# Optimization experiments

Measured on AMD Instinct MI355X. Metric: run time of the kernel, lower is better.

## Reference

```python
import jax, jax.numpy as jnp
import numpy as np

EPS = 1e-06


def setup_inputs() -> dict:
    key = jax.random.key(0)
    k1, k2, k3 = jax.random.split(key, 3)
    B, H, S, D = 4, 16, 4096, 64
    query = jax.random.normal(k1, (B, H, S, D), dtype=jnp.float32)
    key_t = jax.random.normal(k2, (B, H, S, D), dtype=jnp.float32)
    value = jax.random.normal(k3, (B, H, S, D), dtype=jnp.float32)
    return {"query": query, "key": key_t, "value": value}


def _cosformer_features(x, cos_idx, sin_idx):
    # x: [B,H,S,D]; cos_idx/sin_idx: [S,1] -> features [B,H,S,2D]
    x_relu = jax.nn.relu(x)
    return jnp.concatenate([x_relu * cos_idx, x_relu * sin_idx], axis=-1)


def reference(query, key, value):
    B, H, S, D = query.shape
    query = query / jnp.sqrt(jnp.asarray(D, dtype=query.dtype))
    # idx = (pi/2) * [1..S]; angles divided by seq_len
    ang = (jnp.pi / 2) * jnp.arange(1, S + 1, dtype=query.dtype) / S  # [S]
    cos_idx = jnp.cos(ang)[:, None]  # [S,1]
    sin_idx = jnp.sin(ang)[:, None]  # [S,1]
    q_cs = _cosformer_features(query, cos_idx, sin_idx)  # [B,H,S,2D]
    k_cs = _cosformer_features(key, cos_idx, sin_idx)    # [B,H,S,2D]
    # norm: 1 / clamp(q_cs . sum_l(k_cs), eps)
    k_sum = jnp.sum(k_cs, axis=-2)  # [B,H,2D]
    norm = 1.0 / jnp.maximum(jnp.einsum('bhld,bhd->bhl', q_cs, k_sum), EPS)  # [B,H,S]
    # linear attention: KV aggregation then query projection
    kv = jnp.einsum('bhld,bhlm->bhdm', k_cs, value)  # [B,H,2D,D]
    out = jnp.einsum('bhld,bhdm->bhlm', q_cs, kv) * norm[..., None]  # [B,H,S,D]
    return out
```

## Files before the change

kernel.cpp:

```cpp
#include <hip/hip_runtime.h>
#include <hip/hip_bf16.h>
#include <math.h>

#define BHN    64
#define SEQ    4096
#define DIM    64
#define NCHUNK 16
#define CHUNK  (SEQ / NCHUNK)
#define KSTEP  64
#define NIT    (CHUNK / KSTEP)
#define KVF    (128 * DIM)
#define STRIDE_C ((size_t)BHN * KVF + (size_t)BHN * 128)
#define KSBASE ((size_t)BHN * KVF)
#define FRAGH  10240
#define LPAD   72

typedef __bf16 bf16x8v __attribute__((ext_vector_type(8)));
typedef float  f32x4v  __attribute__((ext_vector_type(4)));

__device__ inline f32x4v mfma16(bf16x8v a, bf16x8v b, f32x4v c) {
    return __builtin_amdgcn_mfma_f32_16x16x32_bf16(a, b, c, 0, 0, 0);
}

__device__ inline unsigned pk2(float a, float b) {
    __hip_bfloat162 t(__float2bfloat16(a), __float2bfloat16(b));
    return *(unsigned*)&t;
}

template<int USE_ATOMIC>
__global__ __launch_bounds__(256) void cosformer_kv_mfma(
    const float* __restrict__ K, const float* __restrict__ V,
    float* __restrict__ part)
{
    __shared__ ushort ktc[64][LPAD];
    __shared__ ushort kts[64][LPAD];
    __shared__ ushort vt [64][LPAD];

    const int bh    = blockIdx.x / NCHUNK;
    const int chunk = blockIdx.x % NCHUNK;
    const int row0  = chunk * CHUNK;
    const float* Kb = K + (size_t)bh * SEQ * DIM;
    const float* Vb = V + (size_t)bh * SEQ * DIM;

    const int tid  = threadIdx.x;
    const int ssub = (tid & 31) * 2;
    const int dblk = (tid >> 5) * 8;
    const int lane = tid & 63;
    const int w    = tid >> 6;
    const int frow = lane & 15;
    const int kgrp = lane >> 4;

    f32x4v acc[2][5];
    #pragma unroll
    for (int i = 0; i < 2; ++i)
        #pragma unroll
        for (int t = 0; t < 5; ++t) acc[i][t] = (f32x4v){0.f, 0.f, 0.f, 0.f};

    bf16x8v onef;
    #pragma unroll
    for (int j = 0; j < 8; ++j) onef[j] = (frow == 0) ? (__bf16)1.0f : (__bf16)0.0f;

    float4 kreg[4], vreg[4];

    auto LOADS = [&](int it) {
        const float* kp = Kb + (size_t)(row0 + it * KSTEP + ssub) * DIM + dblk;
        const float* vp = Vb + (size_t)(row0 + it * KSTEP + ssub) * DIM + dblk;
        kreg[0] = *(const float4*)kp;
        kreg[1] = *(const float4*)(kp + 4);
        kreg[2] = *(const float4*)(kp + DIM);
        kreg[3] = *(const float4*)(kp + DIM + 4);
        vreg[0] = *(const float4*)vp;
        vreg[1] = *(const float4*)(vp + 4);
        vreg[2] = *(const float4*)(vp + DIM);
        vreg[3] = *(const float4*)(vp + DIM + 4);
    };

    auto WRITES = [&](int it) {
        const int l0 = row0 + it * KSTEP + ssub;
        const float CC = 1.5707963267948966f / (float)SEQ;
        float s0v, c0, s1v, c1;
        __sincosf(CC * (float)(l0 + 1), &s0v, &c0);
        __sincosf(CC * (float)(l0 + 2), &s1v, &c1);
        float k0[8] = {kreg[0].x, kreg[0].y, kreg[0].z, kreg[0].w,
                       kreg[1].x, kreg[1].y, kreg[1].z, kreg[1].w};
        float k1[8] = {kreg[2].x, kreg[2].y, kreg[2].z, kreg[2].w,
                       kreg[3].x, kreg[3].y, kreg[3].z, kreg[3].w};
        float v0[8] = {vreg[0].x, vreg[0].y, vreg[0].z, vreg[0].w,
                       vreg[1].x, vreg[1].y, vreg[1].z, vreg[1].w};
        float v1[8] = {vreg[2].x, vreg[2].y, vreg[2].z, vreg[2].w,
                       vreg[3].x, vreg[3].y, vreg[3].z, vreg[3].w};
        #pragma unroll
        for (int i = 0; i < 8; ++i) {
            float r0 = fmaxf(k0[i], 0.f), r1 = fmaxf(k1[i], 0.f);
            *(unsigned*)&ktc[dblk + i][ssub] = pk2(r0 * c0,  r1 * c1);
            *(unsigned*)&kts[dblk + i][ssub] = pk2(r0 * s0v, r1 * s1v);
            *(unsigned*)&vt [dblk + i][ssub] = pk2(v0[i],    v1[i]);
        }
    };

    LOADS(0);
    WRITES(0);
    LOADS(1);
    __syncthreads();

    const ushort (*ap)[LPAD] = (w < 2) ? ktc : kts;
    const int d0 = ((2 * w) & 3) * 16 + frow;

    for (int it = 0; it < NIT; ++it) {
        #pragma unroll
        for (int ks = 0; ks < 2; ++ks) {
            const int so = ks * 32 + kgrp * 8;
            bf16x8v a0 = *(const bf16x8v*)&ap[d0][so];
            bf16x8v a1 = *(const bf16x8v*)&ap[d0 + 16][so];
            #pragma unroll
            for (int nt = 0; nt < 4; ++nt) {
                bf16x8v b = *(const bf16x8v*)&vt[nt * 16 + frow][so];
                acc[0][nt] = mfma16(a0, b, acc[0][nt]);
                acc[1][nt] = mfma16(a1, b, acc[1][nt]);
            }
            acc[0][4] = mfma16(a0, onef, acc[0][4]);
            acc[1][4] = mfma16(a1, onef, acc[1][4]);
        }
        __syncthreads();
        if (it + 1 < NIT) {
            WRITES(it + 1);
            if (it + 2 < NIT) LOADS(it + 2);
            __syncthreads();
        }
    }

    if (USE_ATOMIC) {
        float* pb = part + (size_t)bh * KVF;
        float* ps = part + KSBASE + bh * 128;
        #pragma unroll
        for (int mi = 0; mi < 2; ++mi) {
            const int fb = (2 * w + mi) * 16 + kgrp * 4;
            #pragma unroll
            for (int nt = 0; nt < 4; ++nt)
                #pragma unroll
                for (int r = 0; r < 4; ++r)
                    atomicAdd(&pb[(size_t)(fb + r) * DIM + nt * 16 + frow], acc[mi][nt][r]);
            if (frow == 0)
                #pragma unroll
                for (int r = 0; r < 4; ++r) atomicAdd(&ps[fb + r], acc[mi][4][r]);
        }
    } else {
        float* pb = part + STRIDE_C * chunk + (size_t)bh * KVF;
        float* ps = part + STRIDE_C * chunk + KSBASE + bh * 128;
        #pragma unroll
        for (int mi = 0; mi < 2; ++mi) {
            const int fb = (2 * w + mi) * 16 + kgrp * 4;
            #pragma unroll
            for (int nt = 0; nt < 4; ++nt)
                #pragma unroll
                for (int r = 0; r < 4; ++r)
                    pb[(size_t)(fb + r) * DIM + nt * 16 + frow] = acc[mi][nt][r];
            if (frow == 0)
                #pragma unroll
                for (int r = 0; r < 4; ++r) ps[fb + r] = acc[mi][4][r];
        }
    }
}

template<int NC>
__global__ __launch_bounds__(256) void reduce_pack(
    const float* __restrict__ part, __hip_bfloat16* __restrict__ bfrag)
{
    size_t o = (size_t)blockIdx.x * 256 + threadIdx.x;
    float s = 0.f;
    #pragma unroll
    for (int c = 0; c < NC; ++c) s += part[(size_t)c * STRIDE_C + o];
    if (o < KSBASE) {
        int head = (int)(o >> 13);
        int r = (int)(o & 8191);
        int k = r >> 6, n = r & 63;
        int t = n >> 4, ks = k >> 5, lg = (k >> 3) & 3, j = k & 7;
        int lane = lg * 16 + (n & 15);
        bfrag[(size_t)head * FRAGH + (size_t)(((t * 4 + ks) * 64 + lane) * 8 + j)] =
            __float2bfloat16(s);
    } else {
        int r = (int)(o - KSBASE);
        int head = r >> 7, k = r & 127;
        int ks = k >> 5, lg = (k >> 3) & 3, j = k & 7;
        bfrag[(size_t)head * FRAGH + (size_t)(((16 + ks) * 64 + lg * 16) * 8 + j)] =
            __float2bfloat16(s);
    }
}

__global__ __launch_bounds__(256) void cosformer_out_mfma(
    const float* __restrict__ Q, const __hip_bfloat16* __restrict__ bfrag,
    float* __restrict__ out)
{
    __shared__ __hip_bfloat16 sb[FRAGH];
    const int head = blockIdx.x >> 3;
    const int tile = blockIdx.x & 7;
    const int tid  = threadIdx.x;

    {
        const float4* src = (const float4*)(bfrag + (size_t)head * FRAGH);
        float4* dst = (float4*)sb;
        #pragma unroll
        for (int i = 0; i < 5; ++i) dst[tid + 256 * i] = src[tid + 256 * i];
    }

    const int lane = tid & 63;
    const int w    = tid >> 6;
    const int mrow = lane & 15;
    const int kgrp = lane >> 4;

    const float* Qb = Q + (size_t)head * SEQ * DIM;
    float*       Ob = out + (size_t)head * SEQ * DIM;
    const int rowblk = tile * 512;

    float4 qb[2][4];
    #pragma unroll
    for (int m = 0; m < 2; ++m) {
        const float4* qr = (const float4*)(Qb + (size_t)(rowblk + w * 32 + m * 16 + mrow) * DIM);
        qb[m][0] = qr[kgrp * 2];
        qb[m][1] = qr[kgrp * 2 + 1];
        qb[m][2] = qr[8 + kgrp * 2];
        qb[m][3] = qr[8 + kgrp * 2 + 1];
    }

    __syncthreads();

    #pragma unroll
    for (int g = 0; g < 4; ++g) {
        const int base = rowblk + (g * 4 + w) * 32;

        bf16x8v af[2][4];
        #pragma unroll
        for (int m = 0; m < 2; ++m) {
            int arow = base + m * 16 + mrow;
            float ang = 1.5707963267948966f * (float)(arow + 1) / (float)SEQ;
            float sn, cn;
            __sincosf(ang, &sn, &cn);
            float crs = cn * 0.125f, srs = sn * 0.125f;
            float lo[8] = {qb[m][0].x, qb[m][0].y, qb[m][0].z, qb[m][0].w,
                           qb[m][1].x, qb[m][1].y, qb[m][1].z, qb[m][1].w};
            float hi[8] = {qb[m][2].x, qb[m][2].y, qb[m][2].z, qb[m][2].w,
                           qb[m][3].x, qb[m][3].y, qb[m][3].z, qb[m][3].w};
            #pragma unroll
            for (int j = 0; j < 8; ++j) {
                float rl = fmaxf(lo[j], 0.f);
                float rh = fmaxf(hi[j], 0.f);
                af[m][0][j] = (__bf16)(rl * crs);
                af[m][1][j] = (__bf16)(rh * crs);
                af[m][2][j] = (__bf16)(rl * srs);
                af[m][3][j] = (__bf16)(rh * srs);
            }
        }

        if (g < 3) {
            #pragma unroll
            for (int m = 0; m < 2; ++m) {
                const float4* qr = (const float4*)(Qb + (size_t)(rowblk + ((g + 1) * 4 + w) * 32 + m * 16 + mrow) * DIM);
                qb[m][0] = qr[kgrp * 2];
                qb[m][1] = qr[kgrp * 2 + 1];
                qb[m][2] = qr[8 + kgrp * 2];
                qb[m][3] = qr[8 + kgrp * 2 + 1];
            }
        }

        f32x4v acc[2][5];
        #pragma unroll
        for (int m = 0; m < 2; ++m)
            #pragma unroll
            for (int t = 0; t < 5; ++t)
                acc[m][t] = (f32x4v){0.f, 0.f, 0.f, 0.f};

        #pragma unroll
        for (int t = 0; t < 5; ++t)
            #pragma unroll
            for (int ks = 0; ks < 4; ++ks) {
                bf16x8v bf = *(const bf16x8v*)&sb[(size_t)(((t * 4 + ks) * 64 + lane) * 8)];
                acc[0][t] = mfma16(af[0][ks], bf, acc[0][t]);
                acc[1][t] = mfma16(af[1][ks], bf, acc[1][t]);
            }

        #pragma unroll
        for (int m = 0; m < 2; ++m) {
            #pragma unroll
            for (int r = 0; r < 4; ++r) {
                float den = __shfl(acc[m][4][r], lane & 48, 64);
                float invd = 1.0f / fmaxf(den, 1e-6f);
                int row = base + m * 16 + kgrp * 4 + r;
                float* op = Ob + (size_t)row * DIM + mrow;
                op[0]  = acc[m][0][r] * invd;
                op[16] = acc[m][1][r] * invd;
                op[32] = acc[m][2][r] * invd;
                op[48] = acc[m][3][r] * invd;
            }
        }
    }
}

extern "C" void kernel_launch(void* const* d_in, const int* in_sizes, int n_in,
                              void* d_out, int out_size, void* d_ws, size_t ws_size,
                              hipStream_t stream) {
    const float* Q = (const float*)d_in[0];
    const float* K = (const float*)d_in[1];
    const float* V = (const float*)d_in[2];
    float* out = (float*)d_out;
    float* ws  = (float*)d_ws;

    const size_t frag_bytes = (size_t)FRAGH * BHN * sizeof(__hip_bfloat16);
    const size_t need_full  = (size_t)NCHUNK * STRIDE_C * sizeof(float) + frag_bytes;

    if (ws_size >= need_full) {
        float* part = ws;
        __hip_bfloat16* bfrag = (__hip_bfloat16*)(ws + (size_t)NCHUNK * STRIDE_C);
        hipMemsetAsync(bfrag, 0, frag_bytes, stream);
        hipLaunchKernelGGL((cosformer_kv_mfma<0>), dim3(BHN * NCHUNK), dim3(256), 0, stream,
                           K, V, part);
        hipLaunchKernelGGL((reduce_pack<NCHUNK>), dim3((int)(STRIDE_C / 256)), dim3(256), 0, stream,
                           part, bfrag);
        hipLaunchKernelGGL(cosformer_out_mfma, dim3(BHN * 8), dim3(256), 0, stream,
                           Q, bfrag, out);
    } else {
        float* part = ws;
        __hip_bfloat16* bfrag = (__hip_bfloat16*)(ws + STRIDE_C);
        hipMemsetAsync(part, 0, STRIDE_C * sizeof(float), stream);
        hipMemsetAsync(bfrag, 0, frag_bytes, stream);
        hipLaunchKernelGGL((cosformer_kv_mfma<1>), dim3(BHN * NCHUNK), dim3(256), 0, stream,
                           K, V, part);
        hipLaunchKernelGGL((reduce_pack<1>), dim3((int)(STRIDE_C / 256)), dim3(256), 0, stream,
                           part, bfrag);
        hipLaunchKernelGGL(cosformer_out_mfma, dim3(BHN * 8), dim3(256), 0, stream,
                           Q, bfrag, out);
    }
}
```

Measured before the change: 80.91 us.

## Double KV kernel block to 512 threads and XOR-swizzle LDS tiles

The KV aggregation kernel now runs 8 waves per block instead of 4. Each wave computes one 16-row feature tile instead of two, which halves per-thread accumulators and global loads. The transposed LDS tiles are written with an XOR swizzle on the column index, and the MFMA fragment reads use the same swizzle, to cut bank conflicts on the transposed stores. This gives more parallelism and lower register pressure per thread, at the cost of reloading each B fragment for every wave and more barrier participants.

```diff
diff --git a/kernel.cpp b/kernel.cpp
--- a/kernel.cpp
+++ b/kernel.cpp
@@ -27,8 +27,10 @@
     return *(unsigned*)&t;
 }
 
+__device__ inline int swz(int d, int col) { return col ^ (4 * ((d >> 2) & 7)); }
+
 template<int USE_ATOMIC>
-__global__ __launch_bounds__(256) void cosformer_kv_mfma(
+__global__ __launch_bounds__(512) void cosformer_kv_mfma(
     const float* __restrict__ K, const float* __restrict__ V,
     float* __restrict__ part)
 {
@@ -42,59 +44,51 @@
     const float* Kb = K + (size_t)bh * SEQ * DIM;
     const float* Vb = V + (size_t)bh * SEQ * DIM;
 
-    const int tid  = threadIdx.x;
-    const int ssub = (tid & 31) * 2;
-    const int dblk = (tid >> 5) * 8;
+    const int tid = threadIdx.x;
+    const int dq = (tid & 15) * 4;
+    const int g  = tid >> 4;
     const int lane = tid & 63;
     const int w    = tid >> 6;
     const int frow = lane & 15;
     const int kgrp = lane >> 4;
 
-    f32x4v acc[2][5];
-    #pragma unroll
-    for (int i = 0; i < 2; ++i)
-        #pragma unroll
-        for (int t = 0; t < 5; ++t) acc[i][t] = (f32x4v){0.f, 0.f, 0.f, 0.f};
+    f32x4v acc[5];
+    #pragma unroll
+    for (int t = 0; t < 5; ++t) acc[t] = (f32x4v){0.f, 0.f, 0.f, 0.f};
 
     bf16x8v onef;
     #pragma unroll
     for (int j = 0; j < 8; ++j) onef[j] = (frow == 0) ? (__bf16)1.0f : (__bf16)0.0f;
 
-    float4 kreg[4], vreg[4];
+    float4 ka, kb2, va, vb2;
 
     auto LOADS = [&](int it) {
-        const float* kp = Kb + (size_t)(row0 + it * KSTEP + ssub) * DIM + dblk;
-        const float* vp = Vb + (size_t)(row0 + it * KSTEP + ssub) * DIM + dblk;
-        kreg[0] = *(const float4*)kp;
-        kreg[1] = *(const float4*)(kp + 4);
-        kreg[2] = *(const float4*)(kp + DIM);
-        kreg[3] = *(const float4*)(kp + DIM + 4);
-        vreg[0] = *(const float4*)vp;
-        vreg[1] = *(const float4*)(vp + 4);
-        vreg[2] = *(const float4*)(vp + DIM);
-        vreg[3] = *(const float4*)(vp + DIM + 4);
+        const float* kp = Kb + (size_t)(row0 + it * KSTEP + 2 * g) * DIM + dq;
+        const float* vp = Vb + (size_t)(row0 + it * KSTEP + 2 * g) * DIM + dq;
+        ka  = *(const float4*)kp;
+        kb2 = *(const float4*)(kp + DIM);
+        va  = *(const float4*)vp;
+        vb2 = *(const float4*)(vp + DIM);
     };
 
     auto WRITES = [&](int it) {
-        const int l0 = row0 + it * KSTEP + ssub;
+        const int l0 = row0 + it * KSTEP + 2 * g;
         const float CC = 1.5707963267948966f / (float)SEQ;
         float s0v, c0, s1v, c1;
         __sincosf(CC * (float)(l0 + 1), &s0v, &c0);
         __sincosf(CC * (float)(l0 + 2), &s1v, &c1);
-        float k0[8] = {kreg[0].x, kreg[0].y, kreg[0].z, kreg[0].w,
-                       kreg[1].x, kreg[1].y, kreg[1].z, kreg[1].w};
-        float k1[8] = {kreg[2].x, kreg[2].y, kreg[2].z, kreg[2].w,
-                       kreg[3].x, kreg[3].y, kreg[3].z, kreg[3].w};
-        float v0[8] = {vreg[0].x, vreg[0].y, vreg[0].z, vreg[0].w,
-                       vreg[1].x, vreg[1].y, vreg[1].z, vreg[1].w};
-        float v1[8] = {vreg[2].x, vreg[2].y, vreg[2].z, vreg[2].w,
-                       vreg[3].x, vreg[3].y, vreg[3].z, vreg[3].w};
-        #pragma unroll
-        for (int i = 0; i < 8; ++i) {
+        float k0[4] = {ka.x, ka.y, ka.z, ka.w};
+        float k1[4] = {kb2.x, kb2.y, kb2.z, kb2.w};
+        float v0[4] = {va.x, va.y, va.z, va.w};
+        float v1[4] = {vb2.x, vb2.y, vb2.z, vb2.w};
+        #pragma unroll
+        for (int i = 0; i < 4; ++i) {
+            const int d = dq + i;
+            const int c = swz(d, g);
             float r0 = fmaxf(k0[i], 0.f), r1 = fmaxf(k1[i], 0.f);
-            *(unsigned*)&ktc[dblk + i][ssub] = pk2(r0 * c0,  r1 * c1);
-            *(unsigned*)&kts[dblk + i][ssub] = pk2(r0 * s0v, r1 * s1v);
-            *(unsigned*)&vt [dblk + i][ssub] = pk2(v0[i],    v1[i]);
+            ((unsigned*)&ktc[d][0])[c] = pk2(r0 * c0,  r1 * c1);
+            ((unsigned*)&kts[d][0])[c] = pk2(r0 * s0v, r1 * s1v);
+            ((unsigned*)&vt [d][0])[c] = pk2(v0[i],    v1[i]);
         }
     };
 
@@ -103,23 +97,21 @@
     LOADS(1);
     __syncthreads();
 
-    const ushort (*ap)[LPAD] = (w < 2) ? ktc : kts;
-    const int d0 = ((2 * w) & 3) * 16 + frow;
+    const ushort (*ap)[LPAD] = (w < 4) ? ktc : kts;
+    const int d0 = (w & 3) * 16 + frow;
 
     for (int it = 0; it < NIT; ++it) {
         #pragma unroll
         for (int ks = 0; ks < 2; ++ks) {
-            const int so = ks * 32 + kgrp * 8;
-            bf16x8v a0 = *(const bf16x8v*)&ap[d0][so];
-            bf16x8v a1 = *(const bf16x8v*)&ap[d0 + 16][so];
+            const int cb = ks * 16 + kgrp * 4;
+            bf16x8v a = *(const bf16x8v*)&ap[d0][2 * swz(d0, cb)];
             #pragma unroll
             for (int nt = 0; nt < 4; ++nt) {
-                bf16x8v b = *(const bf16x8v*)&vt[nt * 16 + frow][so];
-                acc[0][nt] = mfma16(a0, b, acc[0][nt]);
-                acc[1][nt] = mfma16(a1, b, acc[1][nt]);
-            }
-            acc[0][4] = mfma16(a0, onef, acc[0][4]);
-            acc[1][4] = mfma16(a1, onef, acc[1][4]);
+                const int dn = nt * 16 + frow;
+                bf16x8v b = *(const bf16x8v*)&vt[dn][2 * swz(dn, cb)];
+                acc[nt] = mfma16(a, b, acc[nt]);
+            }
+            acc[4] = mfma16(a, onef, acc[4]);
         }
         __syncthreads();
         if (it + 1 < NIT) {
@@ -129,36 +121,29 @@
         }
     }
 
+    const int fb = w * 16 + kgrp * 4;
     if (USE_ATOMIC) {
         float* pb = part + (size_t)bh * KVF;
         float* ps = part + KSBASE + bh * 128;
         #pragma unroll
-        for (int mi = 0; mi < 2; ++mi) {
-            const int fb = (2 * w + mi) * 16 + kgrp * 4;
-            #pragma unroll
-            for (int nt = 0; nt < 4; ++nt)
-                #pragma unroll
-                for (int r = 0; r < 4; ++r)
-                    atomicAdd(&pb[(size_t)(fb + r) * DIM + nt * 16 + frow], acc[mi][nt][r]);
-            if (frow == 0)
-                #pragma unroll
-                for (int r = 0; r < 4; ++r) atomicAdd(&ps[fb + r], acc[mi][4][r]);
-        }
+        for (int nt = 0; nt < 4; ++nt)
+            #pragma unroll
+            for (int r = 0; r < 4; ++r)
+                atomicAdd(&pb[(size_t)(fb + r) * DIM + nt * 16 + frow], acc[nt][r]);
+        if (frow == 0)
+            #pragma unroll
+            for (int r = 0; r < 4; ++r) atomicAdd(&ps[fb + r], acc[4][r]);
     } else {
         float* pb = part + STRIDE_C * chunk + (size_t)bh * KVF;
         float* ps = part + STRIDE_C * chunk + KSBASE + bh * 128;
         #pragma unroll
-        for (int mi = 0; mi < 2; ++mi) {
-            const int fb = (2 * w + mi) * 16 + kgrp * 4;
-            #pragma unroll
-            for (int nt = 0; nt < 4; ++nt)
-                #pragma unroll
-                for (int r = 0; r < 4; ++r)
-                    pb[(size_t)(fb + r) * DIM + nt * 16 + frow] = acc[mi][nt][r];
-            if (frow == 0)
-                #pragma unroll
-                for (int r = 0; r < 4; ++r) ps[fb + r] = acc[mi][4][r];
-        }
+        for (int nt = 0; nt < 4; ++nt)
+            #pragma unroll
+            for (int r = 0; r < 4; ++r)
+                pb[(size_t)(fb + r) * DIM + nt * 16 + frow] = acc[nt][r];
+        if (frow == 0)
+            #pragma unroll
+            for (int r = 0; r < 4; ++r) ps[fb + r] = acc[4][r];
     }
 }
 
@@ -311,7 +296,7 @@
         float* part = ws;
         __hip_bfloat16* bfrag = (__hip_bfloat16*)(ws + (size_t)NCHUNK * STRIDE_C);
         hipMemsetAsync(bfrag, 0, frag_bytes, stream);
-        hipLaunchKernelGGL((cosformer_kv_mfma<0>), dim3(BHN * NCHUNK), dim3(256), 0, stream,
+        hipLaunchKernelGGL((cosformer_kv_mfma<0>), dim3(BHN * NCHUNK), dim3(512), 0, stream,
                            K, V, part);
         hipLaunchKernelGGL((reduce_pack<NCHUNK>), dim3((int)(STRIDE_C / 256)), dim3(256), 0, stream,
                            part, bfrag);
@@ -322,7 +307,7 @@
         __hip_bfloat16* bfrag = (__hip_bfloat16*)(ws + STRIDE_C);
         hipMemsetAsync(part, 0, STRIDE_C * sizeof(float), stream);
         hipMemsetAsync(bfrag, 0, frag_bytes, stream);
-        hipLaunchKernelGGL((cosformer_kv_mfma<1>), dim3(BHN * NCHUNK), dim3(256), 0, stream,
+        hipLaunchKernelGGL((cosformer_kv_mfma<1>), dim3(BHN * NCHUNK), dim3(512), 0, stream,
                            K, V, part);
         hipLaunchKernelGGL((reduce_pack<1>), dim3((int)(STRIDE_C / 256)), dim3(256), 0, stream,
                            part, bfrag);
```

Measured after the change: 80.15 us. About the same (-0.9%).
